# Kernel optimization log

Hardware: AMD Instinct MI355X
Metric: run time of the kernel (lower is better)

Reference implementation:

```python
import jax, jax.numpy as jnp
import numpy as np

N_NODES = 524288
N_EDGES = 2097152
B = 16384
CONCAT = 128 + 128 + 881  # 1137


def _glorot(key, shape):
    fan_in, fan_out = shape[0], shape[1]
    s = jnp.sqrt(6.0 / (fan_in + fan_out))
    return jax.random.uniform(key, shape, jnp.float32, -s, s)


def setup_inputs() -> dict:
    key = jax.random.key(0)
    ks = jax.random.split(key, 24)
    inp = {
        'drug_x': jax.random.normal(ks[0], (N_NODES, 30), jnp.float32),
        'edge_index': jax.random.randint(ks[1], (2, N_EDGES), 0, N_NODES, jnp.int32),
        'batch': jnp.sort(jax.random.randint(ks[2], (N_NODES,), 0, B, jnp.int32)),
        'protein_x': jax.random.normal(ks[3], (B, 979), jnp.float32),
        'fppubchem': jax.random.uniform(ks[4], (B, 881), jnp.float32),
        # GCN layers (PyG GCNConv: linear no-bias, bias added after aggregation)
        'W1': _glorot(ks[5], (30, 64)), 'b1': jnp.zeros((64,), jnp.float32),
        'W2': _glorot(ks[6], (64, 64)), 'b2': jnp.zeros((64,), jnp.float32),
        'W3': _glorot(ks[7], (64, 64)), 'b3': jnp.zeros((64,), jnp.float32),
        'fc_drug_w': _glorot(ks[8], (64, 128)), 'fc_drug_b': jnp.zeros((128,), jnp.float32),
        'fc_prot_w': _glorot(ks[9], (979, 128)), 'fc_prot_b': jnp.zeros((128,), jnp.float32),
        'fc1_w': _glorot(ks[10], (CONCAT, 512)), 'fc1_b': jnp.zeros((512,), jnp.float32),
        'fc2_w': _glorot(ks[11], (512, 256)), 'fc2_b': jnp.zeros((256,), jnp.float32),
        'fc3_w': _glorot(ks[12], (256, 1)), 'fc3_b': jnp.zeros((1,), jnp.float32),
    }
    return inp


def _gcn_layer(x, W, b, src, dst, deg_inv_sqrt, n_nodes):
    # x' = D^-1/2 (A+I) D^-1/2 (x W) + b   (src/dst already include self-loops)
    h = x @ W
    norm = deg_inv_sqrt[src] * deg_inv_sqrt[dst]  # [E+N]
    msg = h[src] * norm[:, None]
    out = jax.ops.segment_sum(msg, dst, num_segments=n_nodes)
    return out + b


def reference(drug_x, edge_index, batch, protein_x, fppubchem,
              W1, b1, W2, b2, W3, b3,
              fc_drug_w, fc_drug_b, fc_prot_w, fc_prot_b,
              fc1_w, fc1_b, fc2_w, fc2_b, fc3_w, fc3_b):
    n = drug_x.shape[0]
    loops = jnp.arange(n, dtype=edge_index.dtype)
    src = jnp.concatenate([edge_index[0], loops])
    dst = jnp.concatenate([edge_index[1], loops])
    deg = jax.ops.segment_sum(jnp.ones_like(src, jnp.float32), dst, num_segments=n)
    deg_inv_sqrt = jnp.where(deg > 0, jax.lax.rsqrt(jnp.maximum(deg, 1.0)), 0.0)

    h = jax.nn.relu(_gcn_layer(drug_x, W1, b1, src, dst, deg_inv_sqrt, n))
    h = jax.nn.relu(_gcn_layer(h, W2, b2, src, dst, deg_inv_sqrt, n))
    h = jax.nn.relu(_gcn_layer(h, W3, b3, src, dst, deg_inv_sqrt, n))

    # global mean pool over graphs
    nb = fppubchem.shape[0]
    sums = jax.ops.segment_sum(h, batch, num_segments=nb)
    cnts = jax.ops.segment_sum(jnp.ones((n,), jnp.float32), batch, num_segments=nb)
    pooled = sums / jnp.maximum(cnts, 1.0)[:, None]

    drug = jax.nn.relu(pooled @ fc_drug_w + fc_drug_b)
    prot = jax.nn.relu(protein_x @ fc_prot_w + fc_prot_b)
    comb = jnp.concatenate([drug, prot, fppubchem], axis=1)

    # fresh LayerNorm (weight=1, bias=0); dropout treated as identity (eval/deterministic)
    mu = jnp.mean(comb, axis=-1, keepdims=True)
    var = jnp.mean((comb - mu) ** 2, axis=-1, keepdims=True)
    comb = (comb - mu) * jax.lax.rsqrt(var + 1e-5)

    comb = jax.nn.relu(comb @ fc1_w + fc1_b)
    comb = jax.nn.relu(comb @ fc2_w + fc2_b)
    return comb @ fc3_w + fc3_b
```

## Files before the change

### kernel.cpp

```cpp
#include <hip/hip_runtime.h>
#include <hip/hip_bf16.h>

#define CONCAT_F 1137
#define CONCAT_P 1152
#define PROT_K 979
#define PROT_P 992

typedef __attribute__((ext_vector_type(8))) short bf16x8;
typedef __attribute__((ext_vector_type(4))) float f32x4;

static __device__ __forceinline__ float bfu2f(unsigned short u) {
  return __uint_as_float(((unsigned)u) << 16);
}
static __device__ __forceinline__ unsigned short f2bfu(float v) {
  __hip_bfloat16 t = __float2bfloat16(v);
  unsigned short u;
  __builtin_memcpy(&u, &t, 2);
  return u;
}

__global__ void k_count(const int* __restrict__ dst, int* __restrict__ rs, int E) {
  int e = blockIdx.x * blockDim.x + threadIdx.x;
  if (e < E) atomicAdd(&rs[dst[e]], 1);
}

__global__ void k_disk(const int* __restrict__ cnt, float* __restrict__ dis, int n) {
  int i = blockIdx.x * blockDim.x + threadIdx.x;
  if (i < n) dis[i] = rsqrtf(1.0f + (float)cnt[i]);
}

__global__ void k_scan_p1(const int* __restrict__ cnt, int* __restrict__ part, int n) {
  __shared__ int red[256];
  int tid = threadIdx.x;
  long base = (long)blockIdx.x * 1024 + tid * 4;
  int s = 0;
#pragma unroll
  for (int i = 0; i < 4; ++i) {
    long j = base + i;
    if (j < n) s += cnt[j];
  }
  red[tid] = s;
  __syncthreads();
  for (int off = 128; off; off >>= 1) {
    if (tid < off) red[tid] += red[tid + off];
    __syncthreads();
  }
  if (tid == 0) part[blockIdx.x] = red[0];
}

__global__ void k_scan_p2(int* __restrict__ part, int nb) {
  __shared__ int a[1024], b_[1024];
  int t = threadIdx.x;
  a[t] = (t < nb) ? part[t] : 0;
  __syncthreads();
  int* s = a;
  int* d = b_;
  for (int off = 1; off < 1024; off <<= 1) {
    d[t] = s[t] + ((t >= off) ? s[t - off] : 0);
    __syncthreads();
    int* tmp = s;
    s = d;
    d = tmp;
  }
  if (t < nb) part[t] = (t == 0) ? 0 : s[t - 1];
}

__global__ void k_scan_p3(int* __restrict__ rs, const int* __restrict__ part, int n) {
  __shared__ int a[256], b_[256];
  int tid = threadIdx.x;
  long base = (long)blockIdx.x * 1024 + tid * 4;
  int v[4];
#pragma unroll
  for (int i = 0; i < 4; ++i) {
    long j = base + i;
    v[i] = (j < n) ? rs[j] : 0;
  }
  a[tid] = v[0] + v[1] + v[2] + v[3];
  __syncthreads();
  int* s = a;
  int* d = b_;
  for (int off = 1; off < 256; off <<= 1) {
    d[tid] = s[tid] + ((tid >= off) ? s[tid - off] : 0);
    __syncthreads();
    int* t2 = s;
    s = d;
    d = t2;
  }
  int run = part[blockIdx.x] + ((tid == 0) ? 0 : s[tid - 1]);
#pragma unroll
  for (int i = 0; i < 4; ++i) {
    long j = base + i;
    if (j < n) {
      rs[j] = run;
      run += v[i];
    }
  }
}

__global__ void k_scatter(const int* __restrict__ src, const int* __restrict__ dst,
                          int* __restrict__ rs, int* __restrict__ csr, int E) {
  int e = blockIdx.x * blockDim.x + threadIdx.x;
  if (e < E) {
    int pos = atomicAdd(&rs[dst[e]], 1);
    csr[pos] = src[e];
  }
}

template <int K, bool ACT>
__global__ __launch_bounds__(256) void k_mm(const void* __restrict__ Xv,
                                            const float* __restrict__ W,
                                            const float* __restrict__ bprev,
                                            const float* __restrict__ dis,
                                            unsigned short* __restrict__ M, int n) {
  __shared__ __align__(16) float hT[K][68];
  __shared__ __align__(16) float Ws[K * 64];
  __shared__ float disS[64];
  int tid = threadIdx.x;
  int rb = blockIdx.x * 64;
  for (int j = tid; j < K * 16; j += 256) ((float4*)Ws)[j] = ((const float4*)W)[j];
  if (tid < 64) disS[tid] = (rb + tid < n) ? dis[rb + tid] : 0.0f;
  __syncthreads();
  if constexpr (ACT) {
    const unsigned short* X = (const unsigned short*)Xv;
    int k = tid & 63;
    float bk = bprev[k];
#pragma unroll
    for (int r = tid >> 6; r < 64; r += 4) {
      float h = 0.0f;
      if (rb + r < n) {
        float raw = bfu2f(X[(long)(rb + r) * 64 + k]);
        h = fmaxf(fmaf(raw, disS[r], bk), 0.0f);
      }
      hT[k][r] = h;
    }
  } else {
    const float* X = (const float*)Xv;
    for (int idx = tid; idx < 64 * K; idx += 256) {
      int r = idx / K, k = idx - r * K;
      hT[k][r] = (rb + r < n) ? X[(long)(rb + r) * K + k] : 0.0f;
    }
  }
  __syncthreads();
  int rt = (tid & 15) * 4;
  int ct = (tid >> 4) * 4;
  float acc[4][4] = {};
#pragma unroll 5
  for (int k = 0; k < K; ++k) {
    float4 xr = *(const float4*)&hT[k][rt];
    float4 wr = *(const float4*)&Ws[k * 64 + ct];
    float xa[4] = {xr.x, xr.y, xr.z, xr.w};
    float wa[4] = {wr.x, wr.y, wr.z, wr.w};
#pragma unroll
    for (int i = 0; i < 4; ++i)
#pragma unroll
      for (int j = 0; j < 4; ++j) acc[i][j] = fmaf(xa[i], wa[j], acc[i][j]);
  }
#pragma unroll
  for (int i = 0; i < 4; ++i) {
    int row = rb + rt + i;
    if (row >= n) break;
    float dv = disS[rt + i];
    ushort4 pk;
    pk.x = f2bfu(acc[i][0] * dv);
    pk.y = f2bfu(acc[i][1] * dv);
    pk.z = f2bfu(acc[i][2] * dv);
    pk.w = f2bfu(acc[i][3] * dv);
    *(ushort4*)&M[(long)row * 64 + ct] = pk;
  }
}

__global__ __launch_bounds__(256) void k_mmg(const unsigned short* __restrict__ H,
                                             const float* __restrict__ W,
                                             const float* __restrict__ dis,
                                             unsigned short* __restrict__ M, int n) {
  __shared__ __align__(16) unsigned short As[64 * 64];
  __shared__ __align__(16) unsigned short Bt[64 * 64];
  const int tid = threadIdx.x;
  const int bm = blockIdx.x * 64;
  {
    int row = tid >> 2;
    const unsigned short* src = H + (size_t)(bm + row) * 64;
    bool ok = (bm + row) < n;
#pragma unroll
    for (int p = 0; p < 2; ++p) {
      int c = (tid & 3) + p * 4;
      bf16x8 v;
      if (ok) v = *(const bf16x8*)(src + c * 8);
      else v = bf16x8{0, 0, 0, 0, 0, 0, 0, 0};
      int off = (row * 128 + c * 16) ^ ((row & 7) << 4);
      *(bf16x8*)((char*)As + off) = v;
    }
  }
  {
    int nn = tid & 63, k0 = (tid >> 6) * 16;
    bf16x8 v0, v1;
#pragma unroll
    for (int i = 0; i < 8; ++i) v0[i] = (short)f2bfu(W[(size_t)(k0 + i) * 64 + nn]);
#pragma unroll
    for (int i = 0; i < 8; ++i) v1[i] = (short)f2bfu(W[(size_t)(k0 + 8 + i) * 64 + nn]);
    int off0 = (nn * 128 + k0 * 2) ^ ((nn & 7) << 4);
    int off1 = (nn * 128 + (k0 + 8) * 2) ^ ((nn & 7) << 4);
    *(bf16x8*)((char*)Bt + off0) = v0;
    *(bf16x8*)((char*)Bt + off1) = v1;
  }
  __syncthreads();
  const int lane = tid & 63, wid = tid >> 6;
  const int kb = lane >> 4, fr = lane & 15;
  f32x4 acc[4];
#pragma unroll
  for (int i = 0; i < 4; ++i) acc[i] = f32x4{0.f, 0.f, 0.f, 0.f};
  const int ar = wid * 16 + fr;
#pragma unroll
  for (int kc = 0; kc < 2; ++kc) {
    int aoff = (ar * 128 + kc * 64 + kb * 16) ^ ((ar & 7) << 4);
    bf16x8 a = *(const bf16x8*)((char*)As + aoff);
#pragma unroll
    for (int ni = 0; ni < 4; ++ni) {
      int nr = ni * 16 + fr;
      int boff = (nr * 128 + kc * 64 + kb * 16) ^ ((nr & 7) << 4);
      bf16x8 b = *(const bf16x8*)((char*)Bt + boff);
      acc[ni] = __builtin_amdgcn_mfma_f32_16x16x32_bf16(a, b, acc[ni], 0, 0, 0);
    }
  }
#pragma unroll
  for (int r = 0; r < 4; ++r) {
    int row = bm + wid * 16 + kb * 4 + r;
    if (row < n) {
      float dv = dis[row];
#pragma unroll
      for (int ni = 0; ni < 4; ++ni)
        M[(size_t)row * 64 + ni * 16 + fr] = f2bfu(acc[ni][r] * dv);
    }
  }
}

__global__ void k_gather_act(const int* __restrict__ rs, const int* __restrict__ csr,
                             const unsigned short* __restrict__ M,
                             const float* __restrict__ dis, const float* __restrict__ bias,
                             unsigned short* __restrict__ H, int n) {
  int w = (int)((blockIdx.x * (long)blockDim.x + threadIdx.x) >> 6);
  int lane = threadIdx.x & 63;
  int grp = lane >> 4, l16 = lane & 15;
  int node = w * 4 + grp;
  bool act = node < n;
  int start = 0, end = 0;
  if (act) {
    start = (node == 0) ? 0 : rs[node - 1];
    end = rs[node];
  }
  float a0 = 0.f, a1 = 0.f, a2 = 0.f, a3 = 0.f;
  float c0 = 0.f, c1 = 0.f, c2 = 0.f, c3 = 0.f;
  if (act) {
    uint2 v = *(const uint2*)(M + (size_t)node * 64 + l16 * 4);
    a0 = bfu2f(v.x & 0xffffu);
    a1 = bfu2f(v.x >> 16);
    a2 = bfu2f(v.y & 0xffffu);
    a3 = bfu2f(v.y >> 16);
  }
  int j = start;
  for (; j + 1 < end; j += 2) {
    int s0 = csr[j], s1 = csr[j + 1];
    uint2 u = *(const uint2*)(M + (size_t)s0 * 64 + l16 * 4);
    uint2 v = *(const uint2*)(M + (size_t)s1 * 64 + l16 * 4);
    a0 += bfu2f(u.x & 0xffffu);
    a1 += bfu2f(u.x >> 16);
    a2 += bfu2f(u.y & 0xffffu);
    a3 += bfu2f(u.y >> 16);
    c0 += bfu2f(v.x & 0xffffu);
    c1 += bfu2f(v.x >> 16);
    c2 += bfu2f(v.y & 0xffffu);
    c3 += bfu2f(v.y >> 16);
  }
  if (j < end) {
    uint2 u = *(const uint2*)(M + (size_t)csr[j] * 64 + l16 * 4);
    a0 += bfu2f(u.x & 0xffffu);
    a1 += bfu2f(u.x >> 16);
    a2 += bfu2f(u.y & 0xffffu);
    a3 += bfu2f(u.y >> 16);
  }
  if (act) {
    float dv = dis[node];
    float4 bb = *(const float4*)(bias + l16 * 4);
    ushort4 o;
    o.x = f2bfu(fmaxf(fmaf(a0 + c0, dv, bb.x), 0.f));
    o.y = f2bfu(fmaxf(fmaf(a1 + c1, dv, bb.y), 0.f));
    o.z = f2bfu(fmaxf(fmaf(a2 + c2, dv, bb.z), 0.f));
    o.w = f2bfu(fmaxf(fmaf(a3 + c3, dv, bb.w), 0.f));
    *(ushort4*)(H + (size_t)node * 64 + l16 * 4) = o;
  }
}

__global__ void k_pool8(const unsigned short* __restrict__ H, const int* __restrict__ batch,
                        float* __restrict__ sums, float* __restrict__ cntf, int n) {
  int w = (int)((blockIdx.x * (long)blockDim.x + threadIdx.x) >> 6);
  int lane = threadIdx.x & 63;
  int r0 = w * 8;
  if (r0 >= n) return;
  int cur = batch[r0];
  float acc = bfu2f(H[(long)r0 * 64 + lane]);
  float c = 1.0f;
  for (int i = 1; i < 8; ++i) {
    int r = r0 + i;
    if (r >= n) break;
    int b = batch[r];
    float v = bfu2f(H[(long)r * 64 + lane]);
    if (b == cur) {
      acc += v;
      c += 1.0f;
    } else {
      unsafeAtomicAdd(&sums[(long)cur * 64 + lane], acc);
      if (lane == 0) unsafeAtomicAdd(&cntf[cur], c);
      cur = b;
      acc = v;
      c = 1.0f;
    }
  }
  unsafeAtomicAdd(&sums[(long)cur * 64 + lane], acc);
  if (lane == 0) unsafeAtomicAdd(&cntf[cur], c);
}

__global__ void k_drugfc(const float* __restrict__ sums, const float* __restrict__ cnt,
                         const float* __restrict__ W, const float* __restrict__ b,
                         float* __restrict__ out, int B) {
  __shared__ float ps[64];
  int row = blockIdx.x;
  int tid = threadIdx.x;
  float inv = 1.0f / fmaxf(cnt[row], 1.0f);
  if (tid < 64) ps[tid] = sums[(long)row * 64 + tid] * inv;
  __syncthreads();
  float acc = b[tid];
#pragma unroll 8
  for (int k = 0; k < 64; ++k) acc = fmaf(ps[k], W[k * 128 + tid], acc);
  out[(long)row * 128 + tid] = fmaxf(acc, 0.0f);
}

__global__ void k_cvt_bf16(const float* __restrict__ X, unsigned short* __restrict__ Y,
                           int Kin, int ldout) {
  int row = blockIdx.x;
  const float* xr = X + (size_t)row * Kin;
  unsigned short* yr = Y + (size_t)row * ldout;
  for (int j = threadIdx.x; j < ldout; j += 256)
    yr[j] = (j < Kin) ? f2bfu(xr[j]) : 0;
}

template <bool SPLIT, typename OT>
__global__ __launch_bounds__(256, 3) void k_gemm2(
    const unsigned short* __restrict__ A, const float* __restrict__ W,
    const float* __restrict__ bias, OT* __restrict__ C,
    int Mrows, int N, int K, int lda, int nsteps, int chunkSteps) {
  __shared__ __align__(16) unsigned short As[2][64 * 32];
  __shared__ __align__(16) unsigned short Bs[2][128 * 32];
  const int tid = threadIdx.x;
  const int lane = tid & 63;
  const int wid = tid >> 6;
  const int bm = blockIdx.x * 64;
  const int bn = blockIdx.y * 128;
  const int kb = lane >> 4, fr = lane & 15;
  const int ss0 = blockIdx.z * chunkSteps;
  const int ss1 = min(nsteps, ss0 + chunkSteps);

  f32x4 acc[8];
#pragma unroll
  for (int j = 0; j < 8; ++j) acc[j] = f32x4{0.f, 0.f, 0.f, 0.f};

  const int ar = wid * 16 + fr;
  const int aOff = (ar * 64 + kb * 16) ^ ((ar & 7) << 4);
  int bOff[8];
#pragma unroll
  for (int ni = 0; ni < 8; ++ni) {
    int nr = ni * 16 + fr;
    bOff[ni] = (nr * 64 + kb * 16) ^ ((nr & 7) << 4);
  }
  const int arow = tid >> 2, ac = tid & 3;
  const int aW = (arow * 64 + ac * 16) ^ ((arow & 7) << 4);
  const int bn_ = tid & 127, bk0 = (tid >> 7) * 2;
  int bW[2];
#pragma unroll
  for (int p = 0; p < 2; ++p) {
    int kbb = bk0 + p;
    bW[p] = (bn_ * 64 + kbb * 16) ^ ((bn_ & 7) << 4);
  }

  bf16x8 pa;
  float pb[2][8];
  const unsigned short* aptr = A + (size_t)(bm + arow) * lda + ac * 8;

#define LOAD_STEP(S)                                              \
  {                                                               \
    int k0 = (S) * 32;                                            \
    pa = *(const bf16x8*)(aptr + k0);                             \
    _Pragma("unroll") for (int p = 0; p < 2; ++p) {               \
      _Pragma("unroll") for (int i = 0; i < 8; ++i) {             \
        int gk = k0 + (bk0 + p) * 8 + i;                          \
        pb[p][i] = (gk < K) ? W[(size_t)gk * N + bn + bn_] : 0.f; \
      }                                                           \
    }                                                             \
  }
#define STORE_STEP(BUF)                                           \
  {                                                               \
    *(bf16x8*)((char*)As[BUF] + aW) = pa;                         \
    _Pragma("unroll") for (int p = 0; p < 2; ++p) {               \
      bf16x8 v;                                                   \
      _Pragma("unroll") for (int i = 0; i < 8; ++i)               \
          v[i] = (short)f2bfu(pb[p][i]);                          \
      *(bf16x8*)((char*)Bs[BUF] + bW[p]) = v;                     \
    }                                                             \
  }

  LOAD_STEP(ss0);
  STORE_STEP(0);
  __syncthreads();
  int cur = 0;
  for (int s = ss0; s < ss1; ++s) {
    bool more = (s + 1 < ss1);
    if (more) LOAD_STEP(s + 1);
    bf16x8 a0 = *(const bf16x8*)((char*)As[cur] + aOff);
#pragma unroll
    for (int ni = 0; ni < 8; ++ni) {
      bf16x8 b = *(const bf16x8*)((char*)Bs[cur] + bOff[ni]);
      acc[ni] = __builtin_amdgcn_mfma_f32_16x16x32_bf16(a0, b, acc[ni], 0, 0, 0);
    }
    if (more) {
      STORE_STEP(cur ^ 1);
      __syncthreads();
      cur ^= 1;
    }
  }
  if constexpr (SPLIT) {
    float* Cz = (float*)C + (size_t)blockIdx.z * Mrows * N;
#pragma unroll
    for (int ni = 0; ni < 8; ++ni)
#pragma unroll
      for (int r = 0; r < 4; ++r) {
        int row = bm + wid * 16 + kb * 4 + r;
        int col = bn + ni * 16 + fr;
        Cz[(size_t)row * N + col] = acc[ni][r];
      }
  } else {
    float bv[8];
#pragma unroll
    for (int ni = 0; ni < 8; ++ni) bv[ni] = bias[bn + ni * 16 + fr];
#pragma unroll
    for (int ni = 0; ni < 8; ++ni)
#pragma unroll
      for (int r = 0; r < 4; ++r) {
        int row = bm + wid * 16 + kb * 4 + r;
        int col = bn + ni * 16 + fr;
        float x = fmaxf(acc[ni][r] + bv[ni], 0.f);
        if constexpr (__hip_internal::is_same<OT, float>::value) {
          C[(size_t)row * N + col] = x;
        } else {
          C[(size_t)row * N + col] = f2bfu(x);
        }
      }
  }
#undef LOAD_STEP
#undef STORE_STEP
}

__global__ void k_concat_ln(const float* __restrict__ drug, const float* __restrict__ protP,
                            const float* __restrict__ bp, const float* __restrict__ fpp,
                            unsigned short* __restrict__ comb, int B) {
  __shared__ float buf[CONCAT_F];
  __shared__ float rs[4], rs2[4];
  int row = blockIdx.x;
  int tid = threadIdx.x;
  const size_t MN = (size_t)B * 128;
  float s = 0.0f, s2 = 0.0f;
  for (int j = tid; j < CONCAT_F; j += 256) {
    float v;
    if (j < 128) {
      v = drug[(long)row * 128 + j];
    } else if (j < 256) {
      int c = j - 128;
      size_t o = (size_t)row * 128 + c;
      float acc = protP[o] + protP[MN + o] + protP[2 * MN + o] + protP[3 * MN + o];
      v = fmaxf(acc + bp[c], 0.0f);
    } else {
      v = fpp[(long)row * 881 + (j - 256)];
    }
    buf[j] = v;
    s += v;
    s2 += v * v;
  }
  for (int o = 32; o; o >>= 1) {
    s += __shfl_down(s, o, 64);
    s2 += __shfl_down(s2, o, 64);
  }
  int lane = tid & 63, wid = tid >> 6;
  if (lane == 0) { rs[wid] = s; rs2[wid] = s2; }
  __syncthreads();
  if (tid == 0) {
    float ts = rs[0] + rs[1] + rs[2] + rs[3];
    float ts2 = rs2[0] + rs2[1] + rs2[2] + rs2[3];
    float mu = ts / (float)CONCAT_F;
    float var = ts2 / (float)CONCAT_F - mu * mu;
    rs[0] = mu;
    rs2[0] = rsqrtf(fmaxf(var, 0.0f) + 1e-5f);
  }
  __syncthreads();
  float mu = rs[0], inv = rs2[0];
  for (int j = tid; j < CONCAT_P; j += 256) {
    unsigned short o = (j < CONCAT_F) ? f2bfu((buf[j] - mu) * inv) : 0;
    comb[(long)row * CONCAT_P + j] = o;
  }
}

__global__ void k_fc3(const float* __restrict__ X, const float* __restrict__ W,
                      const float* __restrict__ bias, float* __restrict__ out, int B) {
  int w = (int)((blockIdx.x * (long)blockDim.x + threadIdx.x) >> 6);
  int lane = threadIdx.x & 63;
  if (w >= B) return;
  float s = 0.0f;
#pragma unroll
  for (int j = 0; j < 4; ++j) s = fmaf(X[(long)w * 256 + lane + j * 64], W[lane + j * 64], s);
  for (int o = 32; o; o >>= 1) s += __shfl_down(s, o, 64);
  if (lane == 0) out[w] = s + bias[0];
}

extern "C" void kernel_launch(void* const* d_in, const int* in_sizes, int n_in,
                              void* d_out, int out_size, void* d_ws, size_t ws_size,
                              hipStream_t stream) {
  const float* drug_x = (const float*)d_in[0];
  const int* ei = (const int*)d_in[1];
  const int* batch = (const int*)d_in[2];
  const float* protein_x = (const float*)d_in[3];
  const float* fpp = (const float*)d_in[4];
  const float* W1 = (const float*)d_in[5];
  const float* b1 = (const float*)d_in[6];
  const float* W2 = (const float*)d_in[7];
  const float* b2 = (const float*)d_in[8];
  const float* W3 = (const float*)d_in[9];
  const float* b3 = (const float*)d_in[10];
  const float* Wd = (const float*)d_in[11];
  const float* bd = (const float*)d_in[12];
  const float* Wp = (const float*)d_in[13];
  const float* bp = (const float*)d_in[14];
  const float* Wf1 = (const float*)d_in[15];
  const float* bf1 = (const float*)d_in[16];
  const float* Wf2 = (const float*)d_in[17];
  const float* bf2 = (const float*)d_in[18];
  const float* Wf3 = (const float*)d_in[19];
  const float* bf3 = (const float*)d_in[20];
  float* out = (float*)d_out;

  const int N = in_sizes[0] / 30;
  const int E = in_sizes[1] / 2;
  const int B = in_sizes[4] / 881;

  int* rs = (int*)d_ws;
  float* dis = (float*)d_ws + ((size_t)N + 1);
  int* csr = (int*)d_ws + (2 * (size_t)N + 1);
  size_t oM = 2 * (size_t)N + 2 + (size_t)E;
  unsigned short* M = (unsigned short*)((float*)d_ws + oM);
  unsigned short* H = M + (size_t)N * 64;
  float* sums = (float*)d_ws + (oM + 64 * (size_t)N);
  float* cntf = sums + (size_t)B * 64;
  int* part = (int*)(cntf + B);
  unsigned short* protbh = (unsigned short*)(part + 1024);
  float* tail = (float*)d_ws;
  float* drug = tail;
  float* protP = drug + (size_t)B * 128;
  unsigned short* combh = (unsigned short*)(protP + 4 * (size_t)B * 128);
  unsigned short* act1h = combh + (size_t)B * CONCAT_P;
  float* act2 = (float*)(act1h + (size_t)B * 512);

  const int* srcIdx = ei;
  const int* dstIdx = ei + E;

  k_cvt_bf16<<<B, 256, 0, stream>>>(protein_x, protbh, PROT_K, PROT_P);

  hipMemsetAsync(rs, 0, ((size_t)N + 1) * sizeof(int), stream);
  k_count<<<(E + 255) / 256, 256, 0, stream>>>(dstIdx, rs, E);
  k_disk<<<(N + 255) / 256, 256, 0, stream>>>(rs, dis, N);
  int NB = (N + 1023) / 1024;
  k_scan_p1<<<NB, 256, 0, stream>>>(rs, part, N);
  k_scan_p2<<<1, 1024, 0, stream>>>(part, NB);
  k_scan_p3<<<NB, 256, 0, stream>>>(rs, part, N);
  k_scatter<<<(E + 255) / 256, 256, 0, stream>>>(srcIdx, dstIdx, rs, csr, E);

  int mmBlocks = (N + 63) / 64;
  int gWaves = (N + 3) / 4;
  int gBlocks = (gWaves + 3) / 4;
  k_mm<30, false><<<mmBlocks, 256, 0, stream>>>(drug_x, W1, nullptr, dis, M, N);
  k_gather_act<<<gBlocks, 256, 0, stream>>>(rs, csr, M, dis, b1, H, N);
  k_mmg<<<mmBlocks, 256, 0, stream>>>(H, W2, dis, M, N);
  k_gather_act<<<gBlocks, 256, 0, stream>>>(rs, csr, M, dis, b2, H, N);
  k_mmg<<<mmBlocks, 256, 0, stream>>>(H, W3, dis, M, N);
  k_gather_act<<<gBlocks, 256, 0, stream>>>(rs, csr, M, dis, b3, H, N);

  hipMemsetAsync(sums, 0, ((size_t)B * 64 + B) * sizeof(float), stream);
  int poolWaves = (N + 7) / 8;
  k_pool8<<<(poolWaves + 3) / 4, 256, 0, stream>>>(H, batch, sums, cntf, N);

  k_drugfc<<<B, 128, 0, stream>>>(sums, cntf, Wd, bd, drug, B);
  k_gemm2<true, float><<<dim3(B / 64, 1, 4), 256, 0, stream>>>(
      protbh, Wp, nullptr, protP, B, 128, PROT_K, PROT_P, 31, 8);
  k_concat_ln<<<B, 256, 0, stream>>>(drug, protP, bp, fpp, combh, B);
  k_gemm2<false, unsigned short><<<dim3(B / 64, 4, 1), 256, 0, stream>>>(
      combh, Wf1, bf1, act1h, B, 512, CONCAT_F, CONCAT_P, 36, 36);
  k_gemm2<false, float><<<dim3(B / 64, 2, 1), 256, 0, stream>>>(
      act1h, Wf2, bf2, act2, B, 256, 512, 512, 16, 16);
  k_fc3<<<(B + 3) / 4, 256, 0, stream>>>(act2, Wf3, bf3, out, B);
}
```

Baseline: 902.8 us.

## Fuse GCN gather-aggregate with next layer's MFMA matmul into one kernel

Merges the neighbor gather, bias and ReLU of layers 1 and 2 with the following bf16 MFMA matmul, so the activated features go straight into shared memory instead of through an intermediate global H buffer. This removes one write and one read of a 524288x64 bf16 tensor per fused layer, plus two kernel launches. In exchange, the gather now runs at 16 nodes per wave with two-way unrolling inside the matmul block, which may change occupancy and latency hiding. It also ping-pongs the M and H buffers, and the CSR scatter now uses nontemporal stores.

```diff
diff --git a/kernel.cpp b/kernel.cpp
--- a/kernel.cpp
+++ b/kernel.cpp
@@ -102,7 +102,7 @@
   int e = blockIdx.x * blockDim.x + threadIdx.x;
   if (e < E) {
     int pos = atomicAdd(&rs[dst[e]], 1);
-    csr[pos] = src[e];
+    __builtin_nontemporal_store(src[e], &csr[pos]);
   }
 }
 
@@ -169,29 +169,16 @@
   }
 }
 
-__global__ __launch_bounds__(256) void k_mmg(const unsigned short* __restrict__ H,
-                                             const float* __restrict__ W,
-                                             const float* __restrict__ dis,
-                                             unsigned short* __restrict__ M, int n) {
+__global__ __launch_bounds__(256) void k_gmm(
+    const int* __restrict__ rs, const int* __restrict__ csr,
+    const unsigned short* __restrict__ Min, const float* __restrict__ dis,
+    const float* __restrict__ bias, const float* __restrict__ W,
+    unsigned short* __restrict__ Mout, int n) {
   __shared__ __align__(16) unsigned short As[64 * 64];
   __shared__ __align__(16) unsigned short Bt[64 * 64];
   const int tid = threadIdx.x;
   const int bm = blockIdx.x * 64;
   {
-    int row = tid >> 2;
-    const unsigned short* src = H + (size_t)(bm + row) * 64;
-    bool ok = (bm + row) < n;
-#pragma unroll
-    for (int p = 0; p < 2; ++p) {
-      int c = (tid & 3) + p * 4;
-      bf16x8 v;
-      if (ok) v = *(const bf16x8*)(src + c * 8);
-      else v = bf16x8{0, 0, 0, 0, 0, 0, 0, 0};
-      int off = (row * 128 + c * 16) ^ ((row & 7) << 4);
-      *(bf16x8*)((char*)As + off) = v;
-    }
-  }
-  {
     int nn = tid & 63, k0 = (tid >> 6) * 16;
     bf16x8 v0, v1;
 #pragma unroll
@@ -203,13 +190,61 @@
     *(bf16x8*)((char*)Bt + off0) = v0;
     *(bf16x8*)((char*)Bt + off1) = v1;
   }
-  __syncthreads();
-  const int lane = tid & 63, wid = tid >> 6;
+  const int lane = tid & 63;
+  const int wv = tid >> 6;
+  const int grp = lane >> 4, l16 = lane & 15;
+  const float4 bb = *(const float4*)(bias + l16 * 4);
+  for (int p = 0; p < 4; ++p) {
+    int local = wv * 16 + p * 4 + grp;
+    int node = bm + local;
+    float a0 = 0.f, a1 = 0.f, a2 = 0.f, a3 = 0.f;
+    float c0 = 0.f, c1 = 0.f, c2 = 0.f, c3 = 0.f;
+    float dv = 0.f;
+    if (node < n) {
+      uint2 v = *(const uint2*)(Min + (size_t)node * 64 + l16 * 4);
+      a0 = bfu2f(v.x & 0xffffu);
+      a1 = bfu2f(v.x >> 16);
+      a2 = bfu2f(v.y & 0xffffu);
+      a3 = bfu2f(v.y >> 16);
+      int start = (node == 0) ? 0 : rs[node - 1];
+      int end = rs[node];
+      int j = start;
+      for (; j + 1 < end; j += 2) {
+        int s0 = csr[j], s1 = csr[j + 1];
+        uint2 u = *(const uint2*)(Min + (size_t)s0 * 64 + l16 * 4);
+        uint2 w2 = *(const uint2*)(Min + (size_t)s1 * 64 + l16 * 4);
+        a0 += bfu2f(u.x & 0xffffu);
+        a1 += bfu2f(u.x >> 16);
+        a2 += bfu2f(u.y & 0xffffu);
+        a3 += bfu2f(u.y >> 16);
+        c0 += bfu2f(w2.x & 0xffffu);
+        c1 += bfu2f(w2.x >> 16);
+        c2 += bfu2f(w2.y & 0xffffu);
+        c3 += bfu2f(w2.y >> 16);
+      }
+      if (j < end) {
+        uint2 u = *(const uint2*)(Min + (size_t)csr[j] * 64 + l16 * 4);
+        a0 += bfu2f(u.x & 0xffffu);
+        a1 += bfu2f(u.x >> 16);
+        a2 += bfu2f(u.y & 0xffffu);
+        a3 += bfu2f(u.y >> 16);
+      }
+      dv = dis[node];
+    }
+    ushort4 h;
+    h.x = f2bfu(fmaxf(fmaf(a0 + c0, dv, bb.x), 0.f));
+    h.y = f2bfu(fmaxf(fmaf(a1 + c1, dv, bb.y), 0.f));
+    h.z = f2bfu(fmaxf(fmaf(a2 + c2, dv, bb.z), 0.f));
+    h.w = f2bfu(fmaxf(fmaf(a3 + c3, dv, bb.w), 0.f));
+    int off = (local * 128 + l16 * 8) ^ ((local & 7) << 4);
+    *(ushort4*)((char*)As + off) = h;
+  }
+  __syncthreads();
   const int kb = lane >> 4, fr = lane & 15;
   f32x4 acc[4];
 #pragma unroll
   for (int i = 0; i < 4; ++i) acc[i] = f32x4{0.f, 0.f, 0.f, 0.f};
-  const int ar = wid * 16 + fr;
+  const int ar = wv * 16 + fr;
 #pragma unroll
   for (int kc = 0; kc < 2; ++kc) {
     int aoff = (ar * 128 + kc * 64 + kb * 16) ^ ((ar & 7) << 4);
@@ -224,12 +259,12 @@
   }
 #pragma unroll
   for (int r = 0; r < 4; ++r) {
-    int row = bm + wid * 16 + kb * 4 + r;
+    int row = bm + wv * 16 + kb * 4 + r;
     if (row < n) {
-      float dv = dis[row];
+      float dvo = dis[row];
 #pragma unroll
       for (int ni = 0; ni < 4; ++ni)
-        M[(size_t)row * 64 + ni * 16 + fr] = f2bfu(acc[ni][r] * dv);
+        Mout[(size_t)row * 64 + ni * 16 + fr] = f2bfu(acc[ni][r] * dvo);
     }
   }
 }
@@ -583,10 +618,8 @@
   int gWaves = (N + 3) / 4;
   int gBlocks = (gWaves + 3) / 4;
   k_mm<30, false><<<mmBlocks, 256, 0, stream>>>(drug_x, W1, nullptr, dis, M, N);
-  k_gather_act<<<gBlocks, 256, 0, stream>>>(rs, csr, M, dis, b1, H, N);
-  k_mmg<<<mmBlocks, 256, 0, stream>>>(H, W2, dis, M, N);
-  k_gather_act<<<gBlocks, 256, 0, stream>>>(rs, csr, M, dis, b2, H, N);
-  k_mmg<<<mmBlocks, 256, 0, stream>>>(H, W3, dis, M, N);
+  k_gmm<<<mmBlocks, 256, 0, stream>>>(rs, csr, M, dis, b1, W2, H, N);
+  k_gmm<<<mmBlocks, 256, 0, stream>>>(rs, csr, H, dis, b2, W3, M, N);
   k_gather_act<<<gBlocks, 256, 0, stream>>>(rs, csr, M, dis, b3, H, N);
 
   hipMemsetAsync(sums, 0, ((size_t)B * 64 + B) * sizeof(float), stream);
```

Result: faster. 878.2 us (-2.7%).
